# Kernel tuning notes

Hardware: AMD Instinct MI355X
Metric: run time of the kernel (lower is better)

Reference implementation:

```python
import jax, jax.numpy as jnp
import numpy as np

ALPHA = 0.2  # LeakyReLU negative slope


def setup_inputs() -> dict:
    key = jax.random.key(0)
    k1, k2, k3, k4 = jax.random.split(key, 4)
    N, IN, OUT = 8192, 512, 256
    x = jax.random.normal(k1, (N, IN), dtype=jnp.float32)
    adj = jnp.zeros((N, N), dtype=jnp.float32)  # accepted but unused by the module
    W = jax.random.normal(k2, (OUT, IN), dtype=jnp.float32) * (1.0 / np.sqrt(IN))
    a1 = jax.random.normal(k3, (OUT,), dtype=jnp.float32) * (1.0 / np.sqrt(OUT))
    a2 = jax.random.normal(k4, (OUT,), dtype=jnp.float32) * (1.0 / np.sqrt(OUT))
    return {"x": x, "adj": adj, "W": W, "a1": a1, "a2": a2}


def reference(x, adj, W, a1, a2):
    # h = tran(x): [N, OUT]
    h = x @ W.T
    # additive GAT scores: e[i, j] = a2 . h_i + a1 . h_j  (from unsqueeze(0)+unsqueeze(1))
    s1 = h @ a1  # [N], att1(h)
    s2 = h @ a2  # [N], att2(h)
    e = s2[:, None] + s1[None, :]  # [N, N]
    e = jnp.where(e > 0, e, ALPHA * e)  # LeakyReLU
    attn = jax.nn.softmax(e, axis=1)  # softmax over dim=1; dropout is identity in eval
    return attn @ h  # [N, OUT]
```

## Files before the change

### kernel.cpp

```cpp
#include <hip/hip_runtime.h>

#define NROW 8192
#define DIN  512
#define DOUT 256
#define NCHUNK 256
#define CLEN 32
#define JCH 8

constexpr size_t OFF_H      = 0;
constexpr size_t OFF_S1     = OFF_H + (size_t)NROW*DOUT*4;
constexpr size_t OFF_S2     = OFF_S1 + NROW*4;
constexpr size_t OFF_S1S    = OFF_S2 + NROW*4;
constexpr size_t OFF_PERM   = OFF_S1S + NROW*4;
constexpr size_t OFF_WHI    = OFF_PERM + NROW*4;
constexpr size_t OFF_WLO    = OFF_WHI + NROW*4;
constexpr size_t OFF_PRELOS = OFF_WLO + NROW*4;
constexpr size_t OFF_SUFHIS = OFF_PRELOS + 33024;
constexpr size_t OFF_MISC   = OFF_SUFHIS + 33024;
constexpr size_t OFF_PC     = OFF_MISC + 256;
constexpr size_t OFF_TLO    = OFF_PC + (size_t)JCH*NROW*4;
constexpr size_t OFF_THI    = OFF_TLO + (size_t)NCHUNK*DOUT*4;
constexpr size_t OFF_OLO    = OFF_THI + (size_t)NCHUNK*DOUT*4;
constexpr size_t OFF_OHI    = OFF_OLO + (size_t)NCHUNK*DOUT*4;
constexpr size_t OFF_TOTHI  = OFF_OHI + (size_t)NCHUNK*DOUT*4;
constexpr size_t OFF_PRELO  = OFF_TOTHI + 1024;
constexpr size_t OFF_SUFHI  = OFF_PRELO + (size_t)(NROW+1)*DOUT*4;
constexpr size_t WS_NEED    = OFF_SUFHI + (size_t)(NROW+1)*DOUT*4;

__global__ __launch_bounds__(256) void gemm_h(const float* __restrict__ x,
                                              const float* __restrict__ W,
                                              float* __restrict__ h) {
  __shared__ float xs[64][68];
  __shared__ float ws[64][68];
  const int tid = threadIdx.x;
  const int rowBase = blockIdx.x * 64;
  const int colBase = blockIdx.y * 64;
  const int ty = tid >> 4, tx = tid & 15;
  float acc[4][4] = {};
  for (int k0 = 0; k0 < DIN; k0 += 64) {
#pragma unroll
    for (int i = 0; i < 4; ++i) {
      int s = i * 256 + tid;
      int r = s >> 4;
      int kk = (s & 15) << 2;
      float4 v = *(const float4*)(x + (size_t)(rowBase + r) * DIN + k0 + kk);
      xs[kk + 0][r] = v.x; xs[kk + 1][r] = v.y; xs[kk + 2][r] = v.z; xs[kk + 3][r] = v.w;
      float4 u = *(const float4*)(W + (size_t)(colBase + r) * DIN + k0 + kk);
      ws[kk + 0][r] = u.x; ws[kk + 1][r] = u.y; ws[kk + 2][r] = u.z; ws[kk + 3][r] = u.w;
    }
    __syncthreads();
#pragma unroll
    for (int kk = 0; kk < 64; ++kk) {
      float4 av = *(const float4*)&xs[kk][ty << 2];
      float4 bv = *(const float4*)&ws[kk][tx << 2];
      float a[4] = {av.x, av.y, av.z, av.w};
      float b[4] = {bv.x, bv.y, bv.z, bv.w};
#pragma unroll
      for (int r = 0; r < 4; ++r)
#pragma unroll
        for (int c = 0; c < 4; ++c) acc[r][c] = fmaf(a[r], b[c], acc[r][c]);
    }
    __syncthreads();
  }
#pragma unroll
  for (int r = 0; r < 4; ++r) {
    float4 o = make_float4(acc[r][0], acc[r][1], acc[r][2], acc[r][3]);
    *(float4*)(h + (size_t)(rowBase + (ty << 2) + r) * DOUT + colBase + (tx << 2)) = o;
  }
}

__global__ __launch_bounds__(256) void reduce_s(const float* __restrict__ h,
                                                const float* __restrict__ a1,
                                                const float* __restrict__ a2,
                                                float* __restrict__ s1,
                                                float* __restrict__ s2) {
  const int wave = threadIdx.x >> 6, lane = threadIdx.x & 63;
  const int i = blockIdx.x * 4 + wave;
  float4 hv = *(const float4*)(h + (size_t)i * DOUT + (lane << 2));
  float4 A1 = *(const float4*)(a1 + (lane << 2));
  float4 A2 = *(const float4*)(a2 + (lane << 2));
  float d1 = hv.x * A1.x + hv.y * A1.y + hv.z * A1.z + hv.w * A1.w;
  float d2 = hv.x * A2.x + hv.y * A2.y + hv.z * A2.z + hv.w * A2.w;
#pragma unroll
  for (int off = 32; off > 0; off >>= 1) {
    d1 += __shfl_down(d1, off);
    d2 += __shfl_down(d2, off);
  }
  if (lane == 0) { s1[i] = d1; s2[i] = d2; }
}

__global__ __launch_bounds__(256) void rank_partial(const float* __restrict__ s1,
                                                    int* __restrict__ pc) {
  __shared__ float sj[1024];
  const int t = threadIdx.x;
  const int ib = blockIdx.x, jc = blockIdx.y;
  const int j0 = jc * 1024;
  *(float4*)&sj[t << 2] = *(const float4*)(s1 + j0 + (t << 2));
  const int i = ib * 256 + t;
  const float v = s1[i];
  __syncthreads();
  int cnt = 0;
#pragma unroll 4
  for (int q = 0; q < 256; ++q) {
    float4 sv = *(const float4*)&sj[q << 2];
    int jg = j0 + (q << 2);
    cnt += (int)(sv.x < v) + (int)((sv.x == v) & (jg + 0 < i));
    cnt += (int)(sv.y < v) + (int)((sv.y == v) & (jg + 1 < i));
    cnt += (int)(sv.z < v) + (int)((sv.z == v) & (jg + 2 < i));
    cnt += (int)(sv.w < v) + (int)((sv.w == v) & (jg + 3 < i));
  }
  pc[jc * NROW + i] = cnt;
}

__global__ __launch_bounds__(256) void scatter_rank(const float* __restrict__ s1,
                                                    const int* __restrict__ pc,
                                                    float* __restrict__ s1s,
                                                    int* __restrict__ perm) {
  const int i = blockIdx.x * 256 + threadIdx.x;
  int r = 0;
#pragma unroll
  for (int jc = 0; jc < JCH; ++jc) r += pc[jc * NROW + i];
  s1s[r] = s1[i];
  perm[r] = i;
}

__global__ __launch_bounds__(1024) void scan_exp(const float* __restrict__ s1s,
                                                 float* __restrict__ w_hi,
                                                 float* __restrict__ w_lo,
                                                 float* __restrict__ prelo_s,
                                                 float* __restrict__ sufhi_s,
                                                 float* __restrict__ misc) {
  __shared__ float tt[1024];
  const int t = threadIdx.x;
  const float M1 = s1s[NROW - 1];
  float kv[8];
  {
    float4 r1 = *(const float4*)(s1s + 8 * t);
    float4 r2 = *(const float4*)(s1s + 8 * t + 4);
    kv[0] = r1.x; kv[1] = r1.y; kv[2] = r1.z; kv[3] = r1.w;
    kv[4] = r2.x; kv[5] = r2.y; kv[6] = r2.z; kv[7] = r2.w;
  }

  float wl[8];
  float loc = 0.f;
#pragma unroll
  for (int e = 0; e < 8; ++e) { wl[e] = __expf(0.2f * (kv[e] - M1)); loc += wl[e]; }
  tt[t] = loc;
  __syncthreads();
  for (int off = 1; off < 1024; off <<= 1) {
    float v = (t >= off) ? tt[t - off] : 0.f;
    __syncthreads();
    tt[t] += v;
    __syncthreads();
  }
  float run = (t > 0) ? tt[t - 1] : 0.f;
#pragma unroll
  for (int e = 0; e < 8; ++e) {
    int j = 8 * t + e;
    prelo_s[j] = run;
    w_lo[j] = wl[e];
    run += wl[e];
  }
  if (t == 1023) prelo_s[NROW] = run;
  __syncthreads();

  float wh[8];
  loc = 0.f;
#pragma unroll
  for (int e = 0; e < 8; ++e) { wh[e] = __expf(kv[e] - M1); loc += wh[e]; }
  tt[t] = loc;
  __syncthreads();
  for (int off = 1; off < 1024; off <<= 1) {
    float v = (t >= off) ? tt[t - off] : 0.f;
    __syncthreads();
    tt[t] += v;
    __syncthreads();
  }
  float total = tt[1023];
  run = (t > 0) ? tt[t - 1] : 0.f;
#pragma unroll
  for (int e = 0; e < 8; ++e) {
    int j = 8 * t + e;
    sufhi_s[j] = total - run;
    w_hi[j] = wh[e];
    run += wh[e];
  }
  if (t == 1023) sufhi_s[NROW] = 0.f;
  if (t == 0) misc[0] = M1;
}

__global__ __launch_bounds__(256) void chunk_totals(const float* __restrict__ h,
                                                    const int* __restrict__ perm,
                                                    const float* __restrict__ w_hi,
                                                    const float* __restrict__ w_lo,
                                                    float* __restrict__ T_lo,
                                                    float* __restrict__ T_hi) {
  const int d = threadIdx.x, b = blockIdx.x;
  const int j0 = b * CLEN;
  float tlo = 0.f, thi = 0.f;
#pragma unroll
  for (int e = 0; e < CLEN; e += 4) {
    int4 p4 = *(const int4*)(perm + j0 + e);
    float4 wl4 = *(const float4*)(w_lo + j0 + e);
    float4 wh4 = *(const float4*)(w_hi + j0 + e);
    float h0 = h[(size_t)p4.x * DOUT + d];
    float h1 = h[(size_t)p4.y * DOUT + d];
    float h2 = h[(size_t)p4.z * DOUT + d];
    float h3 = h[(size_t)p4.w * DOUT + d];
    tlo += wl4.x * h0 + wl4.y * h1 + wl4.z * h2 + wl4.w * h3;
    thi += wh4.x * h0 + wh4.y * h1 + wh4.z * h2 + wh4.w * h3;
  }
  T_lo[b * DOUT + d] = tlo;
  T_hi[b * DOUT + d] = thi;
}

__global__ __launch_bounds__(256) void scan_chunks(const float* __restrict__ T_lo,
                                                   const float* __restrict__ T_hi,
                                                   float* __restrict__ O_lo,
                                                   float* __restrict__ O_hi,
                                                   float* __restrict__ TotHi,
                                                   float* __restrict__ PreLo,
                                                   float* __restrict__ SufHi) {
  const int d = threadIdx.x;
  float rl = 0.f, rh = 0.f;
#pragma unroll 8
  for (int b = 0; b < NCHUNK; ++b) {
    O_lo[b * DOUT + d] = rl; rl += T_lo[b * DOUT + d];
    O_hi[b * DOUT + d] = rh; rh += T_hi[b * DOUT + d];
  }
  TotHi[d] = rh;
  PreLo[(size_t)NROW * DOUT + d] = rl;
  SufHi[(size_t)NROW * DOUT + d] = 0.f;
}

__global__ __launch_bounds__(256) void write_prefix(const float* __restrict__ h,
                                                    const int* __restrict__ perm,
                                                    const float* __restrict__ w_hi,
                                                    const float* __restrict__ w_lo,
                                                    const float* __restrict__ O_lo,
                                                    const float* __restrict__ O_hi,
                                                    const float* __restrict__ TotHi,
                                                    float* __restrict__ PreLo,
                                                    float* __restrict__ SufHi) {
  const int d = threadIdx.x, b = blockIdx.x;
  float rl = O_lo[b * DOUT + d], rh = O_hi[b * DOUT + d];
  const float tot = TotHi[d];
  const int j0 = b * CLEN;
#pragma unroll
  for (int e = 0; e < CLEN; e += 4) {
    int4 p4 = *(const int4*)(perm + j0 + e);
    float4 wl4 = *(const float4*)(w_lo + j0 + e);
    float4 wh4 = *(const float4*)(w_hi + j0 + e);
    float h0 = h[(size_t)p4.x * DOUT + d];
    float h1 = h[(size_t)p4.y * DOUT + d];
    float h2 = h[(size_t)p4.z * DOUT + d];
    float h3 = h[(size_t)p4.w * DOUT + d];
    size_t j = (size_t)(j0 + e);
    PreLo[(j + 0) * DOUT + d] = rl; SufHi[(j + 0) * DOUT + d] = tot - rh;
    rl += wl4.x * h0; rh += wh4.x * h0;
    PreLo[(j + 1) * DOUT + d] = rl; SufHi[(j + 1) * DOUT + d] = tot - rh;
    rl += wl4.y * h1; rh += wh4.y * h1;
    PreLo[(j + 2) * DOUT + d] = rl; SufHi[(j + 2) * DOUT + d] = tot - rh;
    rl += wl4.z * h2; rh += wh4.z * h2;
    PreLo[(j + 3) * DOUT + d] = rl; SufHi[(j + 3) * DOUT + d] = tot - rh;
    rl += wl4.w * h3; rh += wh4.w * h3;
  }
}

__global__ __launch_bounds__(256) void finalize(const float* __restrict__ s2,
                                                const float* __restrict__ s1s,
                                                const float* __restrict__ misc,
                                                const float* __restrict__ PreLo,
                                                const float* __restrict__ SufHi,
                                                const float* __restrict__ prelo_s,
                                                const float* __restrict__ sufhi_s,
                                                float* __restrict__ out) {
  const int wave = threadIdx.x >> 6, lane = threadIdx.x & 63;
  const int i = blockIdx.x * 4 + wave;
  const float c = s2[i];
  const float M1 = misc[0];
  const float tval = -c;
  int lo = 0, hi = NROW;
  while (lo < hi) {
    int mid = (lo + hi) >> 1;
    if (s1s[mid] <= tval) lo = mid + 1; else hi = mid;
  }
  const int k = lo;
  const float u = c + M1;
  const float m = fmaxf(u, 0.2f * u);
  const float fh = __expf(u - m);
  const float fl = __expf(0.2f * u - m);
  const float den = fh * sufhi_s[k] + fl * prelo_s[k];
  const float inv = 1.f / den;
  float4 A = *(const float4*)(SufHi + (size_t)k * DOUT + (lane << 2));
  float4 B = *(const float4*)(PreLo + (size_t)k * DOUT + (lane << 2));
  float4 o;
  o.x = (fh * A.x + fl * B.x) * inv;
  o.y = (fh * A.y + fl * B.y) * inv;
  o.z = (fh * A.z + fl * B.z) * inv;
  o.w = (fh * A.w + fl * B.w) * inv;
  *(float4*)(out + (size_t)i * DOUT + (lane << 2)) = o;
}

extern "C" void kernel_launch(void* const* d_in, const int* in_sizes, int n_in,
                              void* d_out, int out_size, void* d_ws, size_t ws_size,
                              hipStream_t stream) {
  const float* x  = (const float*)d_in[0];
  const float* W  = (const float*)d_in[2];
  const float* a1 = (const float*)d_in[3];
  const float* a2 = (const float*)d_in[4];
  float* out = (float*)d_out;

  char* ws = (char*)d_ws;
  if (ws_size < WS_NEED) ws = (char*)d_in[1];

  float* h        = (float*)(ws + OFF_H);
  float* s1       = (float*)(ws + OFF_S1);
  float* s2       = (float*)(ws + OFF_S2);
  float* s1s      = (float*)(ws + OFF_S1S);
  int*   perm     = (int*)  (ws + OFF_PERM);
  float* w_hi     = (float*)(ws + OFF_WHI);
  float* w_lo     = (float*)(ws + OFF_WLO);
  float* prelo_s  = (float*)(ws + OFF_PRELOS);
  float* sufhi_s  = (float*)(ws + OFF_SUFHIS);
  float* misc     = (float*)(ws + OFF_MISC);
  int*   pc       = (int*)  (ws + OFF_PC);
  float* T_lo     = (float*)(ws + OFF_TLO);
  float* T_hi     = (float*)(ws + OFF_THI);
  float* O_lo     = (float*)(ws + OFF_OLO);
  float* O_hi     = (float*)(ws + OFF_OHI);
  float* TotHi    = (float*)(ws + OFF_TOTHI);
  float* PreLo    = (float*)(ws + OFF_PRELO);
  float* SufHi    = (float*)(ws + OFF_SUFHI);

  gemm_h<<<dim3(NROW / 64, DOUT / 64), 256, 0, stream>>>(x, W, h);
  reduce_s<<<NROW / 4, 256, 0, stream>>>(h, a1, a2, s1, s2);
  rank_partial<<<dim3(NROW / 256, JCH), 256, 0, stream>>>(s1, pc);
  scatter_rank<<<NROW / 256, 256, 0, stream>>>(s1, pc, s1s, perm);
  scan_exp<<<1, 1024, 0, stream>>>(s1s, w_hi, w_lo, prelo_s, sufhi_s, misc);
  chunk_totals<<<NCHUNK, 256, 0, stream>>>(h, perm, w_hi, w_lo, T_lo, T_hi);
  scan_chunks<<<1, 256, 0, stream>>>(T_lo, T_hi, O_lo, O_hi, TotHi, PreLo, SufHi);
  write_prefix<<<NCHUNK, 256, 0, stream>>>(h, perm, w_hi, w_lo, O_lo, O_hi, TotHi, PreLo, SufHi);
  finalize<<<NROW / 4, 256, 0, stream>>>(s2, s1s, misc, PreLo, SufHi, prelo_s, sufhi_s, out);
}
```

Before: 410.0 us.

## Fuse attention score dot products into GEMM epilogue and drop single-block chunk scan

Computes s1/s2 in the GEMM epilogue via warp shuffles and atomicAdd into zeroed buffers, removing the separate reduce_s pass over h. Replaces the single-block sequential scan_chunks kernel by having each write_prefix block redundantly sum all chunk totals before and after its own chunk. This trades a serial one-block kernel and a launch for redundant reads of the T arrays per block, plus a memset and atomics whose summation order is nondeterministic.

```diff
diff --git a/kernel.cpp b/kernel.cpp
--- a/kernel.cpp
+++ b/kernel.cpp
@@ -20,16 +20,17 @@
 constexpr size_t OFF_PC     = OFF_MISC + 256;
 constexpr size_t OFF_TLO    = OFF_PC + (size_t)JCH*NROW*4;
 constexpr size_t OFF_THI    = OFF_TLO + (size_t)NCHUNK*DOUT*4;
-constexpr size_t OFF_OLO    = OFF_THI + (size_t)NCHUNK*DOUT*4;
-constexpr size_t OFF_OHI    = OFF_OLO + (size_t)NCHUNK*DOUT*4;
-constexpr size_t OFF_TOTHI  = OFF_OHI + (size_t)NCHUNK*DOUT*4;
-constexpr size_t OFF_PRELO  = OFF_TOTHI + 1024;
+constexpr size_t OFF_PRELO  = OFF_THI + (size_t)NCHUNK*DOUT*4;
 constexpr size_t OFF_SUFHI  = OFF_PRELO + (size_t)(NROW+1)*DOUT*4;
 constexpr size_t WS_NEED    = OFF_SUFHI + (size_t)(NROW+1)*DOUT*4;
 
 __global__ __launch_bounds__(256) void gemm_h(const float* __restrict__ x,
                                               const float* __restrict__ W,
-                                              float* __restrict__ h) {
+                                              const float* __restrict__ a1,
+                                              const float* __restrict__ a2,
+                                              float* __restrict__ h,
+                                              float* __restrict__ s1,
+                                              float* __restrict__ s2) {
   __shared__ float xs[64][68];
   __shared__ float ws[64][68];
   const int tid = threadIdx.x;
@@ -67,26 +68,23 @@
     float4 o = make_float4(acc[r][0], acc[r][1], acc[r][2], acc[r][3]);
     *(float4*)(h + (size_t)(rowBase + (ty << 2) + r) * DOUT + colBase + (tx << 2)) = o;
   }
-}
-
-__global__ __launch_bounds__(256) void reduce_s(const float* __restrict__ h,
-                                                const float* __restrict__ a1,
-                                                const float* __restrict__ a2,
-                                                float* __restrict__ s1,
-                                                float* __restrict__ s2) {
-  const int wave = threadIdx.x >> 6, lane = threadIdx.x & 63;
-  const int i = blockIdx.x * 4 + wave;
-  float4 hv = *(const float4*)(h + (size_t)i * DOUT + (lane << 2));
-  float4 A1 = *(const float4*)(a1 + (lane << 2));
-  float4 A2 = *(const float4*)(a2 + (lane << 2));
-  float d1 = hv.x * A1.x + hv.y * A1.y + hv.z * A1.z + hv.w * A1.w;
-  float d2 = hv.x * A2.x + hv.y * A2.y + hv.z * A2.z + hv.w * A2.w;
-#pragma unroll
-  for (int off = 32; off > 0; off >>= 1) {
-    d1 += __shfl_down(d1, off);
-    d2 += __shfl_down(d2, off);
-  }
-  if (lane == 0) { s1[i] = d1; s2[i] = d2; }
+  float4 A1 = *(const float4*)(a1 + colBase + (tx << 2));
+  float4 A2 = *(const float4*)(a2 + colBase + (tx << 2));
+#pragma unroll
+  for (int r = 0; r < 4; ++r) {
+    float p1 = acc[r][0] * A1.x + acc[r][1] * A1.y + acc[r][2] * A1.z + acc[r][3] * A1.w;
+    float p2 = acc[r][0] * A2.x + acc[r][1] * A2.y + acc[r][2] * A2.z + acc[r][3] * A2.w;
+#pragma unroll
+    for (int m = 1; m < 16; m <<= 1) {
+      p1 += __shfl_xor(p1, m);
+      p2 += __shfl_xor(p2, m);
+    }
+    if (tx == 0) {
+      int row = rowBase + (ty << 2) + r;
+      atomicAdd(&s1[row], p1);
+      atomicAdd(&s2[row], p2);
+    }
+  }
 }
 
 __global__ __launch_bounds__(256) void rank_partial(const float* __restrict__ s1,
@@ -214,56 +212,53 @@
   T_hi[b * DOUT + d] = thi;
 }
 
-__global__ __launch_bounds__(256) void scan_chunks(const float* __restrict__ T_lo,
-                                                   const float* __restrict__ T_hi,
-                                                   float* __restrict__ O_lo,
-                                                   float* __restrict__ O_hi,
-                                                   float* __restrict__ TotHi,
-                                                   float* __restrict__ PreLo,
-                                                   float* __restrict__ SufHi) {
-  const int d = threadIdx.x;
-  float rl = 0.f, rh = 0.f;
-#pragma unroll 8
-  for (int b = 0; b < NCHUNK; ++b) {
-    O_lo[b * DOUT + d] = rl; rl += T_lo[b * DOUT + d];
-    O_hi[b * DOUT + d] = rh; rh += T_hi[b * DOUT + d];
-  }
-  TotHi[d] = rh;
-  PreLo[(size_t)NROW * DOUT + d] = rl;
-  SufHi[(size_t)NROW * DOUT + d] = 0.f;
-}
-
 __global__ __launch_bounds__(256) void write_prefix(const float* __restrict__ h,
                                                     const int* __restrict__ perm,
                                                     const float* __restrict__ w_hi,
                                                     const float* __restrict__ w_lo,
-                                                    const float* __restrict__ O_lo,
-                                                    const float* __restrict__ O_hi,
-                                                    const float* __restrict__ TotHi,
+                                                    const float* __restrict__ T_lo,
+                                                    const float* __restrict__ T_hi,
                                                     float* __restrict__ PreLo,
                                                     float* __restrict__ SufHi) {
   const int d = threadIdx.x, b = blockIdx.x;
-  float rl = O_lo[b * DOUT + d], rh = O_hi[b * DOUT + d];
-  const float tot = TotHi[d];
+  float rl = 0.f, tail = 0.f;
+#pragma unroll 8
+  for (int p = 0; p < NCHUNK; ++p) {
+    float vl = T_lo[p * DOUT + d];
+    float vh = T_hi[p * DOUT + d];
+    rl   += (p < b) ? vl : 0.f;
+    tail += (p > b) ? vh : 0.f;
+  }
   const int j0 = b * CLEN;
+  float hv[CLEN];
+  float wlv[CLEN], whv[CLEN];
+  float ownHi = 0.f;
 #pragma unroll
   for (int e = 0; e < CLEN; e += 4) {
     int4 p4 = *(const int4*)(perm + j0 + e);
     float4 wl4 = *(const float4*)(w_lo + j0 + e);
     float4 wh4 = *(const float4*)(w_hi + j0 + e);
-    float h0 = h[(size_t)p4.x * DOUT + d];
-    float h1 = h[(size_t)p4.y * DOUT + d];
-    float h2 = h[(size_t)p4.z * DOUT + d];
-    float h3 = h[(size_t)p4.w * DOUT + d];
+    hv[e + 0] = h[(size_t)p4.x * DOUT + d];
+    hv[e + 1] = h[(size_t)p4.y * DOUT + d];
+    hv[e + 2] = h[(size_t)p4.z * DOUT + d];
+    hv[e + 3] = h[(size_t)p4.w * DOUT + d];
+    wlv[e + 0] = wl4.x; wlv[e + 1] = wl4.y; wlv[e + 2] = wl4.z; wlv[e + 3] = wl4.w;
+    whv[e + 0] = wh4.x; whv[e + 1] = wh4.y; whv[e + 2] = wh4.z; whv[e + 3] = wh4.w;
+    ownHi += wh4.x * hv[e] + wh4.y * hv[e + 1] + wh4.z * hv[e + 2] + wh4.w * hv[e + 3];
+  }
+  float shb = tail + ownHi;
+  float preh = 0.f;
+#pragma unroll
+  for (int e = 0; e < CLEN; ++e) {
     size_t j = (size_t)(j0 + e);
-    PreLo[(j + 0) * DOUT + d] = rl; SufHi[(j + 0) * DOUT + d] = tot - rh;
-    rl += wl4.x * h0; rh += wh4.x * h0;
-    PreLo[(j + 1) * DOUT + d] = rl; SufHi[(j + 1) * DOUT + d] = tot - rh;
-    rl += wl4.y * h1; rh += wh4.y * h1;
-    PreLo[(j + 2) * DOUT + d] = rl; SufHi[(j + 2) * DOUT + d] = tot - rh;
-    rl += wl4.z * h2; rh += wh4.z * h2;
-    PreLo[(j + 3) * DOUT + d] = rl; SufHi[(j + 3) * DOUT + d] = tot - rh;
-    rl += wl4.w * h3; rh += wh4.w * h3;
+    PreLo[j * DOUT + d] = rl;
+    SufHi[j * DOUT + d] = shb - preh;
+    rl   += wlv[e] * hv[e];
+    preh += whv[e] * hv[e];
+  }
+  if (b == NCHUNK - 1) {
+    PreLo[(size_t)NROW * DOUT + d] = rl;
+    SufHi[(size_t)NROW * DOUT + d] = 0.f;
   }
 }
 
@@ -327,19 +322,16 @@
   int*   pc       = (int*)  (ws + OFF_PC);
   float* T_lo     = (float*)(ws + OFF_TLO);
   float* T_hi     = (float*)(ws + OFF_THI);
-  float* O_lo     = (float*)(ws + OFF_OLO);
-  float* O_hi     = (float*)(ws + OFF_OHI);
-  float* TotHi    = (float*)(ws + OFF_TOTHI);
   float* PreLo    = (float*)(ws + OFF_PRELO);
   float* SufHi    = (float*)(ws + OFF_SUFHI);
 
-  gemm_h<<<dim3(NROW / 64, DOUT / 64), 256, 0, stream>>>(x, W, h);
-  reduce_s<<<NROW / 4, 256, 0, stream>>>(h, a1, a2, s1, s2);
+  hipMemsetAsync(s1, 0, (size_t)2 * NROW * 4, stream);
+
+  gemm_h<<<dim3(NROW / 64, DOUT / 64), 256, 0, stream>>>(x, W, a1, a2, h, s1, s2);
   rank_partial<<<dim3(NROW / 256, JCH), 256, 0, stream>>>(s1, pc);
   scatter_rank<<<NROW / 256, 256, 0, stream>>>(s1, pc, s1s, perm);
   scan_exp<<<1, 1024, 0, stream>>>(s1s, w_hi, w_lo, prelo_s, sufhi_s, misc);
   chunk_totals<<<NCHUNK, 256, 0, stream>>>(h, perm, w_hi, w_lo, T_lo, T_hi);
-  scan_chunks<<<1, 256, 0, stream>>>(T_lo, T_hi, O_lo, O_hi, TotHi, PreLo, SufHi);
-  write_prefix<<<NCHUNK, 256, 0, stream>>>(h, perm, w_hi, w_lo, O_lo, O_hi, TotHi, PreLo, SufHi);
+  write_prefix<<<NCHUNK, 256, 0, stream>>>(h, perm, w_hi, w_lo, T_lo, T_hi, PreLo, SufHi);
   finalize<<<NROW / 4, 256, 0, stream>>>(s2, s1s, misc, PreLo, SufHi, prelo_s, sufhi_s, out);
 }
```

Result: no change. 405.2 us (-1.2%).
